# Performance work log

Hardware: AMD Instinct MI355X
Metric: run time of the kernel (lower is better)

Reference implementation:

```python
import jax, jax.numpy as jnp
import numpy as np

B, LC, LQ, H = 64, 1024, 128, 512
NEG = -1e30


def setup_inputs() -> dict:
    key = jax.random.key(0)
    ks = jax.random.split(key, 12)
    s = 1.0 / np.sqrt(H)
    return {
        "c": jax.random.normal(ks[0], (B, LC, H), jnp.float32),
        "q": jax.random.normal(ks[1], (B, LQ, H), jnp.float32),
        "c_mask": jax.random.randint(ks[2], (B, LC), 0, 2, jnp.int32),
        "q_mask": jax.random.randint(ks[3], (B, LQ), 0, 2, jnp.int32),
        "c_weight": jax.random.normal(ks[4], (H, 1), jnp.float32) * s,
        "q_weight": jax.random.normal(ks[5], (H, 1), jnp.float32) * s,
        "cq_weight": jax.random.normal(ks[6], (1, 1, H), jnp.float32) * s,
        "bias": jnp.zeros((1,), jnp.float32),
        "W1": jax.random.normal(ks[7], (H, H), jnp.float32) * s,
        "b1": jnp.zeros((H,), jnp.float32),
        "W2": jax.random.normal(ks[8], (H, H), jnp.float32) * s,
        "b2": jnp.zeros((H,), jnp.float32),
    }


def reference(c, q, c_mask, q_mask, c_weight, q_weight, cq_weight, bias, W1, b1, W2, b2):
    # --- trilinear similarity (BiDAF eq. 1, memory-efficient form) ---
    s0 = c @ c_weight                                   # [B, LC, 1]
    s1 = jnp.swapaxes(q @ q_weight, 1, 2)               # [B, 1, LQ]
    s2 = jnp.einsum('bch,bqh->bcq', c * cq_weight, q)   # [B, LC, LQ]
    sim = s0 + s1 + s2 + bias

    qm = (q_mask != 0)[:, None, :]   # [B, 1, LQ]
    cm = (c_mask != 0)[:, :, None]   # [B, LC, 1]

    # dual masked softmax (dropout is identity in eval mode)
    s1s = jax.nn.softmax(jnp.where(qm, sim, NEG), axis=2)  # c2q weights
    s2s = jax.nn.softmax(jnp.where(cm, sim, NEG), axis=1)  # q2c weights

    a = s1s @ q                                            # [B, LC, H]
    b = jnp.einsum('bcq,bkq->bck', s1s, s2s) @ c           # [B, LC, H]

    # co-attention branch: qprime = relu(lin2(relu(lin1(q))))
    qp = jax.nn.relu(jax.nn.relu(q @ W1 + b1) @ W2 + b2)   # [B, LQ, H]
    scoat = jnp.einsum('bch,bqh->bcq', c, qp)              # [B, LC, LQ]
    sc1 = jax.nn.softmax(jnp.where(qm, scoat, NEG), axis=2)
    sc2 = jax.nn.softmax(jnp.where(cm, scoat, NEG), axis=1)
    acoat = sc1 @ qp                                       # [B, LC, H]
    bcoat = jnp.einsum('bcq,bch->bqh', sc2, c)             # [B, LQ, H]
    scoat3 = sc1 @ bcoat                                   # [B, LC, H]

    return jnp.concatenate([c, a, c * a, c * b, scoat3, acoat], axis=2)  # [B, LC, 6H]
```

## Files before the change

### kernel.cpp

```cpp
#include <hip/hip_runtime.h>
#include <cstdint>
#include <cstddef>

typedef short    bf16x8 __attribute__((ext_vector_type(8)));
typedef _Float16 f16x8  __attribute__((ext_vector_type(8)));
typedef _Float16 f16x4  __attribute__((ext_vector_type(4)));
typedef float    f32x4  __attribute__((ext_vector_type(4)));

#define NEGV (-1e30f)
#define LDT 40

__device__ __forceinline__ short f2bf(float x){
    union { float f; unsigned u; } v; v.f = x;
    return (short)((v.u + 0x7fffu + ((v.u >> 16) & 1u)) >> 16);
}
__device__ __forceinline__ float bf2f(short h){
    union { float f; unsigned u; } v; v.u = ((unsigned)(unsigned short)h) << 16; return v.f;
}
__device__ __forceinline__ short f2h(float x){
    _Float16 h = (_Float16)x;
    union { _Float16 h; unsigned short u; } v; v.h = h;
    return (short)v.u;
}
__device__ __forceinline__ unsigned packh(float a, float b){
    return (unsigned)(unsigned short)f2h(a) | ((unsigned)(unsigned short)f2h(b) << 16);
}
__device__ __forceinline__ int p64(int x){ return ((x & 3) << 4) | (x >> 2); }

__global__ __launch_bounds__(256)
void k_prep_w(const float* __restrict__ W1, const float* __restrict__ W2,
              short* __restrict__ W1Th, short* __restrict__ W1Tl,
              short* __restrict__ W2Th, short* __restrict__ W2Tl)
{
    int idx = blockIdx.x * 256 + threadIdx.x;
    int w = idx >> 18;
    int e = idx & ((1 << 18) - 1);
    int n = e & 511, k = e >> 9;
    const float* W = w ? W2 : W1;
    float x = W[k * 512 + n];
    short hi = f2bf(x);
    short lo = f2bf(x - bf2f(hi));
    size_t o = (size_t)n * 512 + k;
    if (w) { W2Th[o] = hi; W2Tl[o] = lo; } else { W1Th[o] = hi; W1Tl[o] = lo; }
}

__global__ __launch_bounds__(256)
void k_prep_q(const float* __restrict__ q, const float* __restrict__ qwv,
              const float* __restrict__ cqw, short* __restrict__ q_cq,
              short* __restrict__ qT, float* __restrict__ s1p)
{
    __shared__ short TT[128 * 136];
    __shared__ float qws[128], cqs[128];
    const int t = threadIdx.x;
    const int b = (int)(blockIdx.x >> 2), hb = (int)(blockIdx.x & 3), h0 = hb * 128;
    if (t < 128) { qws[t] = qwv[h0 + t]; cqs[t] = cqw[h0 + t]; }
    __syncthreads();
    #pragma unroll
    for (int it = 0; it < 16; it++) {
        int idx = it * 256 + t;
        int m = idx >> 5, c4 = (idx & 31) * 4;
        float4 v = *(const float4*)(q + ((size_t)b * 128 + m) * 512 + h0 + c4);
        TT[(c4 + 0) * 136 + m] = f2h(v.x);
        TT[(c4 + 1) * 136 + m] = f2h(v.y);
        TT[(c4 + 2) * 136 + m] = f2h(v.z);
        TT[(c4 + 3) * 136 + m] = f2h(v.w);
        uint2 d;
        d.x = packh(v.x * cqs[c4],     v.y * cqs[c4 + 1]);
        d.y = packh(v.z * cqs[c4 + 2], v.w * cqs[c4 + 3]);
        *(uint2*)(q_cq + ((size_t)b * 128 + m) * 512 + h0 + c4) = d;
        float dot = v.x * qws[c4] + v.y * qws[c4 + 1] + v.z * qws[c4 + 2] + v.w * qws[c4 + 3];
        #pragma unroll
        for (int off = 1; off < 32; off <<= 1) dot += __shfl_xor(dot, off);
        if ((t & 31) == 0) s1p[((size_t)b * 4 + hb) * 128 + m] = dot;
    }
    __syncthreads();
    const int h = t >> 1, half = t & 1;
    const int hm = (h & 64) + p64(h & 63);
    short* dst = qT + ((size_t)b * 512 + h0 + hm) * 128 + half * 64;
    #pragma unroll
    for (int j = 0; j < 8; j++)
        *(bf16x8*)(dst + j * 8) = *(const bf16x8*)&TT[h * 136 + half * 64 + j * 8];
}

template<bool WT>
__global__ __launch_bounds__(256)
void k_linear(const float* __restrict__ X, const short* __restrict__ WTh,
              const short* __restrict__ WTl, const float* __restrict__ bias,
              float* __restrict__ Y, short* __restrict__ Yf,
              short* __restrict__ YT)
{
    __shared__ __align__(16) short SMEM[4 * 128 * LDT];
    short* Ah = SMEM;
    short* Al = SMEM + 128 * LDT;
    short* Bh = SMEM + 2 * 128 * LDT;
    short* Bl = SMEM + 3 * 128 * LDT;
    const int t = threadIdx.x;
    const int m0 = (int)(blockIdx.x >> 2) * 128;
    const int n0 = (int)(blockIdx.x & 3) * 128;
    const int lane = t & 63;
    const int wr = (t >> 7) & 1, wc = (t >> 6) & 1;
    const int fr = lane & 15, fg = lane >> 4;
    const int srow = t >> 1, sk = (t & 1) * 16;

    f32x4 acc[4][4] = {};

    float4 fX[4];
    bf16x8 fWh[2], fWl[2];
    bf16x8 hiR[2], loR[2];
    auto load_raw = [&](int k0) {
        const float* src = X + (size_t)(m0 + srow) * 512 + k0 + sk;
        #pragma unroll
        for (int i = 0; i < 4; i++) fX[i] = ((const float4*)src)[i];
        const short* sh = WTh + (size_t)(n0 + srow) * 512 + k0 + sk;
        const short* sl = WTl + (size_t)(n0 + srow) * 512 + k0 + sk;
        fWh[0] = ((const bf16x8*)sh)[0]; fWh[1] = ((const bf16x8*)sh)[1];
        fWl[0] = ((const bf16x8*)sl)[0]; fWl[1] = ((const bf16x8*)sl)[1];
    };
    auto split_cvt = [&]() {
        const float* fv = (const float*)fX;
        short hi[16], lo[16];
        #pragma unroll
        for (int j = 0; j < 16; j++) {
            float x = fv[j];
            short h = f2bf(x);
            hi[j] = h; lo[j] = f2bf(x - bf2f(h));
        }
        hiR[0] = *(bf16x8*)&hi[0]; hiR[1] = *(bf16x8*)&hi[8];
        loR[0] = *(bf16x8*)&lo[0]; loR[1] = *(bf16x8*)&lo[8];
    };

    load_raw(0);
    split_cvt();

    for (int k0 = 0; k0 < 512; k0 += 32) {
        __syncthreads();
        *(bf16x8*)&Ah[srow * LDT + sk]     = hiR[0];
        *(bf16x8*)&Ah[srow * LDT + sk + 8] = hiR[1];
        *(bf16x8*)&Al[srow * LDT + sk]     = loR[0];
        *(bf16x8*)&Al[srow * LDT + sk + 8] = loR[1];
        *(bf16x8*)&Bh[srow * LDT + sk]     = fWh[0];
        *(bf16x8*)&Bh[srow * LDT + sk + 8] = fWh[1];
        *(bf16x8*)&Bl[srow * LDT + sk]     = fWl[0];
        *(bf16x8*)&Bl[srow * LDT + sk + 8] = fWl[1];
        __syncthreads();
        const bool more = (k0 + 32) < 512;
        if (more) load_raw(k0 + 32);
        bf16x8 a_h[4], a_l[4], b_h[4], b_l[4];
        #pragma unroll
        for (int i = 0; i < 4; i++) {
            int ar = (wr * 64 + i * 16 + fr) * LDT + fg * 8;
            int br = (wc * 64 + i * 16 + fr) * LDT + fg * 8;
            a_h[i] = *(const bf16x8*)&Ah[ar];
            a_l[i] = *(const bf16x8*)&Al[ar];
            b_h[i] = *(const bf16x8*)&Bh[br];
            b_l[i] = *(const bf16x8*)&Bl[br];
        }
        #pragma unroll
        for (int mi = 0; mi < 4; mi++)
        #pragma unroll
        for (int ni = 0; ni < 4; ni++) {
            acc[mi][ni] = __builtin_amdgcn_mfma_f32_16x16x32_bf16(a_h[mi], b_h[ni], acc[mi][ni], 0, 0, 0);
            acc[mi][ni] = __builtin_amdgcn_mfma_f32_16x16x32_bf16(a_h[mi], b_l[ni], acc[mi][ni], 0, 0, 0);
            acc[mi][ni] = __builtin_amdgcn_mfma_f32_16x16x32_bf16(a_l[mi], b_h[ni], acc[mi][ni], 0, 0, 0);
        }
        if (more) split_cvt();
    }
    float bv[4];
    #pragma unroll
    for (int ni = 0; ni < 4; ni++) bv[ni] = bias[n0 + wc * 64 + ni * 16 + fr];

    if (!WT) {
        #pragma unroll
        for (int mi = 0; mi < 4; mi++)
        #pragma unroll
        for (int r = 0; r < 4; r++) {
            int row = m0 + wr * 64 + mi * 16 + fg * 4 + r;
            #pragma unroll
            for (int ni = 0; ni < 4; ni++)
                Y[(size_t)row * 512 + n0 + wc * 64 + ni * 16 + fr] =
                    fmaxf(acc[mi][ni][r] + bv[ni], 0.f);
        }
    } else {
        #pragma unroll
        for (int mi = 0; mi < 4; mi++)
        #pragma unroll
        for (int r = 0; r < 4; r++) {
            int row = m0 + wr * 64 + mi * 16 + fg * 4 + r;
            #pragma unroll
            for (int ni = 0; ni < 4; ni++) {
                float v = fmaxf(acc[mi][ni][r] + bv[ni], 0.f);
                size_t o = (size_t)row * 512 + n0 + wc * 64 + ni * 16 + fr;
                Yf[o] = f2h(v);
            }
        }
        __syncthreads();
        short* TT = SMEM;
        #pragma unroll
        for (int mi = 0; mi < 4; mi++)
        #pragma unroll
        for (int r = 0; r < 4; r++) {
            int ml = wr * 64 + mi * 16 + fg * 4 + r;
            #pragma unroll
            for (int ni = 0; ni < 4; ni++)
                TT[(wc * 64 + ni * 16 + fr) * 136 + ml] =
                    f2h(fmaxf(acc[mi][ni][r] + bv[ni], 0.f));
        }
        __syncthreads();
        const int n = t >> 1, half = t & 1;
        const int nm = (n & 64) + p64(n & 63);
        short* dst = YT + ((size_t)(m0 >> 7) * 512 + n0 + nm) * 128 + half * 64;
        #pragma unroll
        for (int j = 0; j < 8; j++)
            *(bf16x8*)(dst + j * 8) = *(const bf16x8*)&TT[n * 136 + half * 64 + j * 8];
    }
}

__global__ __launch_bounds__(256, 2)
void k_att_dual(const float* __restrict__ Cc, const short* __restrict__ B1g,
                const short* __restrict__ B2g, const float* __restrict__ cwv,
                const float* __restrict__ s1pg, const float* __restrict__ biasp,
                const int* __restrict__ qmask, const int* __restrict__ cmask,
                short* __restrict__ c16,
                short* __restrict__ Pr1, short* __restrict__ Pe1, float2* __restrict__ cp1,
                short* __restrict__ Pr2, short* __restrict__ Pe2, float2* __restrict__ cp2)
{
    __shared__ __align__(16) short SM[128 * 136];
    short* Ah  = SM;
    short* B1h = SM + 128 * LDT;
    short* B2h = SM + 2 * 128 * LDT;
    short* TT  = SM;
    __shared__ float red[2][128];
    __shared__ float mrowL[128], rinvL[128], cmaxL[128];
    __shared__ float cws[512];
    __shared__ float s0red[128][2];
    __shared__ float s0L[128], s1L[128];
    __shared__ int qmsL[128], cmsL[128];

    const int t = threadIdx.x;
    const int b  = (int)(blockIdx.x & 63);
    const int ch = (int)(blockIdx.x >> 6);
    const int m0 = ch * 128;
    const int lane = t & 63;
    const int wr = (t >> 7) & 1, wc = (t >> 6) & 1;
    const int fr = lane & 15, fg = lane >> 4;
    const int srow = t >> 1, sk = (t & 1) * 16;

    cws[t] = cwv[t]; cws[t + 256] = cwv[t + 256];
    if (t < 128) {
        qmsL[t] = qmask[b * 128 + t];
        cmsL[t] = cmask[b * 1024 + m0 + t];
        s1L[t] = s1pg[((size_t)b * 4 + 0) * 128 + t] + s1pg[((size_t)b * 4 + 1) * 128 + t]
               + s1pg[((size_t)b * 4 + 2) * 128 + t] + s1pg[((size_t)b * 4 + 3) * 128 + t];
    }

    const size_t aoff = ((size_t)b * 1024 + m0 + srow) * 512;
    const size_t boff = ((size_t)b * 128 + srow) * 512;
    float s0part = 0.f;
    f32x4 acc1[4][4] = {}, acc2[4][4] = {};

    float4 fA[4];
    uint4 fB1[2], fB2[2];
    bf16x8 hvR[2];
    auto load_raw = [&](int k0) {
        const float* src = Cc + aoff + k0 + sk;
        #pragma unroll
        for (int i = 0; i < 4; i++) fA[i] = ((const float4*)src)[i];
        fB1[0] = *(const uint4*)(B1g + boff + k0 + sk);
        fB1[1] = *(const uint4*)(B1g + boff + k0 + sk + 8);
        fB2[0] = *(const uint4*)(B2g + boff + k0 + sk);
        fB2[1] = *(const uint4*)(B2g + boff + k0 + sk + 8);
    };
    auto cvt_exp = [&](int k0) {
        const float* fv = (const float*)fA;
        short hv[16];
        #pragma unroll
        for (int j = 0; j < 16; j++) {
            float x = fv[j];
            s0part += x * cws[k0 + sk + j];
            hv[j] = f2h(x);
        }
        hvR[0] = *(bf16x8*)&hv[0]; hvR[1] = *(bf16x8*)&hv[8];
        *(bf16x8*)(c16 + aoff + k0 + sk)     = hvR[0];
        *(bf16x8*)(c16 + aoff + k0 + sk + 8) = hvR[1];
    };

    load_raw(0);
    cvt_exp(0);

    for (int k0 = 0; k0 < 512; k0 += 32) {
        __syncthreads();
        *(bf16x8*)&Ah[srow * LDT + sk]      = hvR[0];
        *(bf16x8*)&Ah[srow * LDT + sk + 8]  = hvR[1];
        *(uint4*)&B1h[srow * LDT + sk]      = fB1[0];
        *(uint4*)&B1h[srow * LDT + sk + 8]  = fB1[1];
        *(uint4*)&B2h[srow * LDT + sk]      = fB2[0];
        *(uint4*)&B2h[srow * LDT + sk + 8]  = fB2[1];
        __syncthreads();
        const bool more = (k0 + 32) < 512;
        if (more) load_raw(k0 + 32);
        #pragma unroll
        for (int i = 0; i < 4; i++) {
            f16x8 a_ = *(const f16x8*)&Ah[(wr * 64 + i * 16 + fr) * LDT + fg * 8];
            #pragma unroll
            for (int ni = 0; ni < 4; ni++) {
                int br = (wc * 64 + ni * 16 + fr) * LDT + fg * 8;
                f16x8 b1_ = *(const f16x8*)&B1h[br];
                acc1[i][ni] = __builtin_amdgcn_mfma_f32_16x16x32_f16(a_, b1_, acc1[i][ni], 0, 0, 0);
                f16x8 b2_ = *(const f16x8*)&B2h[br];
                acc2[i][ni] = __builtin_amdgcn_mfma_f32_16x16x32_f16(a_, b2_, acc2[i][ni], 0, 0, 0);
            }
        }
        if (more) cvt_exp(k0 + 32);
    }

    s0red[srow][t & 1] = s0part;
    __syncthreads();
    if (t < 128) s0L[t] = s0red[t][0] + s0red[t][1];
    __syncthreads();
    {
        float b0 = biasp[0];
        #pragma unroll
        for (int mi = 0; mi < 4; mi++)
        #pragma unroll
        for (int r = 0; r < 4; r++) {
            float s0r = s0L[wr * 64 + mi * 16 + fg * 4 + r] + b0;
            #pragma unroll
            for (int ni = 0; ni < 4; ni++)
                acc1[mi][ni][r] += s0r + s1L[wc * 64 + ni * 16 + fr];
        }
    }

    bool qmv[4];
    #pragma unroll
    for (int ni = 0; ni < 4; ni++) qmv[ni] = qmsL[wc * 64 + ni * 16 + fr] != 0;
    bool cmb[4][4];
    #pragma unroll
    for (int mi = 0; mi < 4; mi++)
    #pragma unroll
    for (int r = 0; r < 4; r++) cmb[mi][r] = cmsL[wr * 64 + mi * 16 + fg * 4 + r] != 0;

    auto emit = [&](f32x4 (&acc)[4][4], short* __restrict__ Pr,
                    short* __restrict__ Pe, float2* __restrict__ cpart_g) {
        __syncthreads();
        #pragma unroll
        for (int mi = 0; mi < 4; mi++)
        #pragma unroll
        for (int r = 0; r < 4; r++) {
            float m = NEGV;
            #pragma unroll
            for (int ni = 0; ni < 4; ni++) if (qmv[ni]) m = fmaxf(m, acc[mi][ni][r]);
            #pragma unroll
            for (int off = 1; off < 16; off <<= 1) m = fmaxf(m, __shfl_xor(m, off));
            if (fr == 0) red[wc][wr * 64 + mi * 16 + fg * 4 + r] = m;
        }
        __syncthreads();
        if (t < 128) mrowL[t] = fmaxf(red[0][t], red[1][t]);
        __syncthreads();
        #pragma unroll
        for (int mi = 0; mi < 4; mi++)
        #pragma unroll
        for (int r = 0; r < 4; r++) {
            float mr = mrowL[wr * 64 + mi * 16 + fg * 4 + r];
            float s = 0.f;
            #pragma unroll
            for (int ni = 0; ni < 4; ni++) if (qmv[ni]) s += __expf(acc[mi][ni][r] - mr);
            #pragma unroll
            for (int off = 1; off < 16; off <<= 1) s += __shfl_xor(s, off);
            if (fr == 0) red[wc][wr * 64 + mi * 16 + fg * 4 + r] = s;
        }
        __syncthreads();
        if (t < 128) rinvL[t] = 1.f / (red[0][t] + red[1][t]);
        __syncthreads();
        #pragma unroll
        for (int mi = 0; mi < 4; mi++)
        #pragma unroll
        for (int r = 0; r < 4; r++) {
            int rowl = wr * 64 + mi * 16 + fg * 4 + r;
            float mr = mrowL[rowl], iv = rinvL[rowl];
            size_t obase = ((size_t)b * 1024 + m0 + rowl) * 128;
            #pragma unroll
            for (int ni = 0; ni < 4; ni++) {
                float o = qmv[ni] ? __expf(acc[mi][ni][r] - mr) * iv : 0.f;
                Pr[obase + wc * 64 + ni * 16 + fr] = f2h(o);
            }
        }
        float cpart[4];
        #pragma unroll
        for (int ni = 0; ni < 4; ni++) {
            float m = NEGV;
            #pragma unroll
            for (int mi = 0; mi < 4; mi++)
            #pragma unroll
            for (int r = 0; r < 4; r++) if (cmb[mi][r]) m = fmaxf(m, acc[mi][ni][r]);
            m = fmaxf(m, __shfl_xor(m, 16));
            m = fmaxf(m, __shfl_xor(m, 32));
            cpart[ni] = m;
        }
        if (fg == 0) {
            #pragma unroll
            for (int ni = 0; ni < 4; ni++) red[wr][wc * 64 + ni * 16 + fr] = cpart[ni];
        }
        __syncthreads();
        if (t < 128) cmaxL[t] = fmaxf(red[0][t], red[1][t]);
        __syncthreads();
        #pragma unroll
        for (int ni = 0; ni < 4; ni++) {
            const int q = wc * 64 + ni * 16 + fr;
            float cm = cmaxL[q];
            float s = 0.f;
            #pragma unroll
            for (int mi = 0; mi < 4; mi++)
            #pragma unroll
            for (int r = 0; r < 4; r++) {
                int rloc = wr * 64 + mi * 16 + fg * 4 + r;
                float e = cmb[mi][r] ? __expf(acc[mi][ni][r] - cm) : 0.f;
                s += e;
                TT[q * 136 + rloc] = f2h(e);
            }
            s += __shfl_xor(s, 16);
            s += __shfl_xor(s, 32);
            cpart[ni] = s;
        }
        __syncthreads();
        if (fg == 0) {
            #pragma unroll
            for (int ni = 0; ni < 4; ni++) red[wr][wc * 64 + ni * 16 + fr] = cpart[ni];
        }
        __syncthreads();
        {
            const int q2 = t >> 1, half = t & 1;
            short* dst = Pe + ((size_t)b * 128 + q2) * 1024 + m0 + half * 64;
            #pragma unroll
            for (int j = 0; j < 8; j++)
                *(bf16x8*)(dst + j * 8) = *(const bf16x8*)&TT[q2 * 136 + half * 64 + j * 8];
        }
        if (t < 128) cpart_g[((size_t)b * 8 + ch) * 128 + t] = make_float2(cmaxL[t], red[0][t] + red[1][t]);
    };

    emit(acc1, Pr1, Pe1, cp1);
    emit(acc2, Pr2, Pe2, cp2);
}

__global__ __launch_bounds__(256)
void k_kgemm2(const short* __restrict__ A1, const short* __restrict__ A2,
              const short* __restrict__ C16, const float2* __restrict__ cpS,
              const float2* __restrict__ cpC, short* __restrict__ Y1T,
              short* __restrict__ Y2T)
{
    __shared__ __align__(16) short Bs[2][64 * LDT];
    __shared__ __align__(16) short TT[64 * 136];
    __shared__ float wtr[2][8][128];
    __shared__ float fin[2][128];
    const int t = threadIdx.x;
    const int b  = (int)(blockIdx.x & 63);
    const int n0 = (int)(blockIdx.x >> 6) * 64;
    const int lane = t & 63;
    const int w  = t >> 6;
    const int wr = w >> 1, wc = w & 1;
    const int fr = lane & 15, fg = lane >> 4;
    const int n4 = (t & 15) * 4, kk2 = (t >> 4) * 2;

    {
        const int tb = t >> 7, qq = t & 127;
        const float2* cp = tb ? cpC : cpS;
        float2 pc[8];
        #pragma unroll
        for (int c2 = 0; c2 < 8; c2++) pc[c2] = cp[((size_t)b * 8 + c2) * 128 + qq];
        float Mg = NEGV;
        #pragma unroll
        for (int c2 = 0; c2 < 8; c2++) Mg = fmaxf(Mg, pc[c2].x);
        float Sg = 0.f;
        #pragma unroll
        for (int c2 = 0; c2 < 8; c2++) Sg += pc[c2].y * __expf(pc[c2].x - Mg);
        const float clampv = Mg - 60.f;
        float mh[8];
        #pragma unroll
        for (int c2 = 0; c2 < 8; c2++) mh[c2] = fmaxf(pc[c2].x, clampv);
        wtr[tb][0][qq] = 1.f;
        #pragma unroll
        for (int c2 = 1; c2 < 8; c2++) wtr[tb][c2][qq] = __expf(mh[c2 - 1] - mh[c2]);
        fin[tb][qq] = (Sg > 0.f) ? __expf(mh[7] - Mg) / Sg : 0.f;
    }

    f32x4 acc1[4][2] = {}, acc2[4][2] = {};

    auto load_e = [&](int k0, uint2* e) {
        const short* p = C16 + ((size_t)b * 1024 + k0 + kk2) * 512 + n0 + n4;
        e[0] = *(const uint2*)(p);
        e[1] = *(const uint2*)(p + 512);
    };
    auto store_b = [&](const uint2* e, int buf) {
        const unsigned short* r0 = (const unsigned short*)&e[0];
        const unsigned short* r1 = (const unsigned short*)&e[1];
        #pragma unroll
        for (int l = 0; l < 4; l++)
            *(unsigned*)&Bs[buf][(n4 + l) * LDT + kk2] = (unsigned)r0[l] | ((unsigned)r1[l] << 16);
    };

    {
        uint2 e[2];
        load_e(0, e);
        store_b(e, 0);
    }
    __syncthreads();

    for (int k0 = 0; k0 < 1024; k0 += 32) {
        const int cur = (k0 >> 5) & 1;
        const bool more = (k0 + 32) < 1024;
        uint2 e[2];
        if (more) load_e(k0 + 32, e);
        if (k0 && (k0 & 127) == 0) {
            const int c2 = k0 >> 7;
            #pragma unroll
            for (int mi = 0; mi < 4; mi++)
            #pragma unroll
            for (int r = 0; r < 4; r++) {
                int qq = wr * 64 + mi * 16 + fg * 4 + r;
                float f1 = wtr[0][c2][qq], f2 = wtr[1][c2][qq];
                #pragma unroll
                for (int ni = 0; ni < 2; ni++) {
                    acc1[mi][ni][r] *= f1;
                    acc2[mi][ni][r] *= f2;
                }
            }
        }
        f16x8 a1[4], a2[4], bg[2];
        #pragma unroll
        for (int i = 0; i < 4; i++) {
            size_t arow = (size_t)(b * 128 + wr * 64 + i * 16 + fr) * 1024 + k0 + fg * 8;
            a1[i] = *(const f16x8*)(A1 + arow);
            a2[i] = *(const f16x8*)(A2 + arow);
        }
        #pragma unroll
        for (int i = 0; i < 2; i++)
            bg[i] = *(const f16x8*)&Bs[cur][(wc * 32 + i * 16 + fr) * LDT + fg * 8];
        #pragma unroll
        for (int mi = 0; mi < 4; mi++)
        #pragma unroll
        for (int ni = 0; ni < 2; ni++) {
            acc1[mi][ni] = __builtin_amdgcn_mfma_f32_16x16x32_f16(a1[mi], bg[ni], acc1[mi][ni], 0, 0, 0);
            acc2[mi][ni] = __builtin_amdgcn_mfma_f32_16x16x32_f16(a2[mi], bg[ni], acc2[mi][ni], 0, 0, 0);
        }
        if (more) store_b(e, cur ^ 1);
        __syncthreads();
    }

    const int n_l = t >> 2, qu = t & 3;
    const int nm = p64(n_l);
    #pragma unroll
    for (int mi = 0; mi < 4; mi++)
    #pragma unroll
    for (int r = 0; r < 4; r++) {
        int ml = wr * 64 + mi * 16 + fg * 4 + r;
        float fs = fin[0][ml];
        #pragma unroll
        for (int ni = 0; ni < 2; ni++)
            TT[(wc * 32 + ni * 16 + fr) * 136 + ml] = f2h(acc1[mi][ni][r] * fs);
    }
    __syncthreads();
    {
        short* dst = Y1T + ((size_t)b * 512 + n0 + nm) * 128 + qu * 32;
        #pragma unroll
        for (int j = 0; j < 4; j++)
            *(bf16x8*)(dst + j * 8) = *(const bf16x8*)&TT[n_l * 136 + qu * 32 + j * 8];
    }
    __syncthreads();
    #pragma unroll
    for (int mi = 0; mi < 4; mi++)
    #pragma unroll
    for (int r = 0; r < 4; r++) {
        int ml = wr * 64 + mi * 16 + fg * 4 + r;
        float fs = fin[1][ml];
        #pragma unroll
        for (int ni = 0; ni < 2; ni++)
            TT[(wc * 32 + ni * 16 + fr) * 136 + ml] = f2h(acc2[mi][ni][r] * fs);
    }
    __syncthreads();
    {
        short* dst = Y2T + ((size_t)b * 512 + n0 + nm) * 128 + qu * 32;
        #pragma unroll
        for (int j = 0; j < 4; j++)
            *(bf16x8*)(dst + j * 8) = *(const bf16x8*)&TT[n_l * 136 + qu * 32 + j * 8];
    }
}

template<bool WITHC>
__global__ __launch_bounds__(256)
void k_epi(const short* __restrict__ Pm, const short* __restrict__ BT1,
           const short* __restrict__ BT2, const short* __restrict__ C16,
           float* __restrict__ out)
{
    const int t = threadIdx.x;
    const int hb = (int)(blockIdx.x & 3);
    const int mb = (int)((blockIdx.x >> 2) & 7);
    const int b  = (int)(blockIdx.x >> 5);
    const int m0 = mb * 128, h0 = hb * 128;
    const int lane = t & 63;
    const int wr = (t >> 7) & 1, wc = (t >> 6) & 1;
    const int fr = lane & 15, fg = lane >> 4;
    f32x4 acc1[4][4] = {}, acc2[4][4] = {};
    const short* Abase  = Pm  + ((size_t)b * 1024 + m0) * 128;
    const short* B1base = BT1 + ((size_t)b * 512 + h0) * 128;
    const short* B2base = BT2 + ((size_t)b * 512 + h0) * 128;
    #pragma unroll
    for (int kk = 0; kk < 4; kk++) {
        const int k0 = kk * 32;
        f16x8 af[4], b1[4], b2[4];
        #pragma unroll
        for (int i = 0; i < 4; i++) {
            af[i] = *(const f16x8*)(Abase  + (size_t)(wr * 64 + i * 16 + fr) * 128 + k0 + fg * 8);
            b1[i] = *(const f16x8*)(B1base + (size_t)(wc * 64 + i * 16 + fr) * 128 + k0 + fg * 8);
            b2[i] = *(const f16x8*)(B2base + (size_t)(wc * 64 + i * 16 + fr) * 128 + k0 + fg * 8);
        }
        #pragma unroll
        for (int mi = 0; mi < 4; mi++)
        #pragma unroll
        for (int ni = 0; ni < 4; ni++) {
            acc1[mi][ni] = __builtin_amdgcn_mfma_f32_16x16x32_f16(af[mi], b1[ni], acc1[mi][ni], 0, 0, 0);
            acc2[mi][ni] = __builtin_amdgcn_mfma_f32_16x16x32_f16(af[mi], b2[ni], acc2[mi][ni], 0, 0, 0);
        }
    }
    const size_t crow_base = (size_t)b * 1024 + m0;
    const int colb = wc * 64 + fr * 4;
    #pragma unroll
    for (int mi = 0; mi < 4; mi++)
    #pragma unroll
    for (int r = 0; r < 4; r++) {
        int rowl = wr * 64 + mi * 16 + fg * 4 + r;
        size_t obase = (crow_base + rowl) * 3072 + h0 + colb;
        float4 av, bv;
        av.x = acc1[mi][0][r]; av.y = acc1[mi][1][r]; av.z = acc1[mi][2][r]; av.w = acc1[mi][3][r];
        bv.x = acc2[mi][0][r]; bv.y = acc2[mi][1][r]; bv.z = acc2[mi][2][r]; bv.w = acc2[mi][3][r];
        if (WITHC) {
            f16x4 cv4 = *(const f16x4*)(C16 + (crow_base + rowl) * 512 + h0 + colb);
            float4 cv;
            cv.x = (float)cv4[0]; cv.y = (float)cv4[1]; cv.z = (float)cv4[2]; cv.w = (float)cv4[3];
            *(float4*)(out + obase) = cv;
            *(float4*)(out + obase + 512) = av;
            float4 ca; ca.x = cv.x * av.x; ca.y = cv.y * av.y; ca.z = cv.z * av.z; ca.w = cv.w * av.w;
            *(float4*)(out + obase + 1024) = ca;
            float4 cb; cb.x = cv.x * bv.x; cb.y = cv.y * bv.y; cb.z = cv.z * bv.z; cb.w = cv.w * bv.w;
            *(float4*)(out + obase + 1536) = cb;
        } else {
            *(float4*)(out + obase + 2048) = bv;
            *(float4*)(out + obase + 2560) = av;
        }
    }
}

extern "C" void kernel_launch(void* const* d_in, const int* in_sizes, int n_in,
                              void* d_out, int out_size, void* d_ws, size_t ws_size,
                              hipStream_t stream)
{
    const float* c     = (const float*)d_in[0];
    const float* q     = (const float*)d_in[1];
    const int*   cmask = (const int*)d_in[2];
    const int*   qmask = (const int*)d_in[3];
    const float* cwv   = (const float*)d_in[4];
    const float* qwv   = (const float*)d_in[5];
    const float* cqw   = (const float*)d_in[6];
    const float* bias  = (const float*)d_in[7];
    const float* W1    = (const float*)d_in[8];
    const float* b1    = (const float*)d_in[9];
    const float* W2    = (const float*)d_in[10];
    const float* b2    = (const float*)d_in[11];
    float* out = (float*)d_out;

    char* ws = (char*)d_ws;
    size_t off = 0;
    auto alloc = [&](size_t bytes) -> char* {
        char* p = ws + off;
        off = (off + bytes + 255) & ~(size_t)255;
        return p;
    };
    short* w1th = (short*)alloc(512 * 512 * 2);
    short* w1tl = (short*)alloc(512 * 512 * 2);
    short* w2th = (short*)alloc(512 * 512 * 2);
    short* w2tl = (short*)alloc(512 * 512 * 2);
    float* s1p  = (float*)alloc(64 * 4 * 128 * 4);
    short* q_cq = (short*)alloc((size_t)64 * 128 * 512 * 2);
    short* qT   = (short*)alloc((size_t)64 * 512 * 128 * 2);
    float* z1   = (float*)alloc((size_t)8192 * 512 * 4);
    short* qp_f = (short*)alloc((size_t)8192 * 512 * 2);
    short* qpT  = (short*)alloc((size_t)64 * 512 * 128 * 2);
    short* c16  = (short*)alloc((size_t)64 * 1024 * 512 * 2);
    float2* colpartS = (float2*)alloc((size_t)64 * 8 * 128 * 8);
    float2* colpartC = (float2*)alloc((size_t)64 * 8 * 128 * 8);
    short* s1s  = (short*)alloc((size_t)64 * 1024 * 128 * 2);
    short* s2sT = (short*)alloc((size_t)64 * 128 * 1024 * 2);
    short* sc1  = (short*)alloc((size_t)64 * 1024 * 128 * 2);
    short* sc2T = (short*)alloc((size_t)64 * 128 * 1024 * 2);
    short* binT = (short*)z1;
    short* bcoT = ((short*)z1) + (size_t)64 * 512 * 128;

    k_prep_w<<<2048, 256, 0, stream>>>(W1, W2, w1th, w1tl, w2th, w2tl);
    k_prep_q<<<256, 256, 0, stream>>>(q, qwv, cqw, q_cq, qT, s1p);
    k_linear<false><<<256, 256, 0, stream>>>(q, w1th, w1tl, b1, z1, nullptr, nullptr);
    k_linear<true><<<256, 256, 0, stream>>>(z1, w2th, w2tl, b2, nullptr, qp_f, qpT);

    k_att_dual<<<512, 256, 0, stream>>>(
        c, q_cq, qp_f, cwv, s1p, bias, qmask, cmask, c16,
        s1s, s2sT, colpartS, sc1, sc2T, colpartC);

    k_kgemm2<<<512, 256, 0, stream>>>(s2sT, sc2T, c16, colpartS, colpartC, binT, bcoT);

    k_epi<true><<<2048, 256, 0, stream>>>(s1s, qT, binT, c16, out);
    k_epi<false><<<2048, 256, 0, stream>>>(sc1, qpT, bcoT, nullptr, out);
}
```

Baseline: 572.3 us.

## Merge epilogue GEMM kernels into one launch with smaller tiles and sequential accumulators

Replaces the two templated epilogue launches with a single kernel of 8192 blocks that picks the attention or co-attention branch from the low bit of the block index. The M tile is halved to 64 rows, and the two GEMMs per block run one after another, each with a 2x4 accumulator set instead of two simultaneous 4x4 sets. This cuts accumulator register pressure to raise occupancy, removes one launch, and lets both branches' stores interleave. In exchange the c16 tile is loaded twice in part 0 and the A fragments are reloaded for each GEMM.

```diff
diff --git a/kernel.cpp b/kernel.cpp
--- a/kernel.cpp
+++ b/kernel.cpp
@@ -584,66 +584,109 @@
     }
 }
 
-template<bool WITHC>
 __global__ __launch_bounds__(256)
-void k_epi(const short* __restrict__ Pm, const short* __restrict__ BT1,
-           const short* __restrict__ BT2, const short* __restrict__ C16,
-           float* __restrict__ out)
+void k_epi2(const short* __restrict__ s1s, const short* __restrict__ qT,
+            const short* __restrict__ binT, const short* __restrict__ c16,
+            const short* __restrict__ sc1, const short* __restrict__ qpT,
+            const short* __restrict__ bcoT, float* __restrict__ out)
 {
+    const int bid = (int)blockIdx.x;
+    const int part = bid & 1;
+    const int lb = bid >> 1;
+    const int hb = lb & 3, mb = (lb >> 2) & 15, b = lb >> 6;
+    const int m0 = mb * 64, h0 = hb * 128;
     const int t = threadIdx.x;
-    const int hb = (int)(blockIdx.x & 3);
-    const int mb = (int)((blockIdx.x >> 2) & 7);
-    const int b  = (int)(blockIdx.x >> 5);
-    const int m0 = mb * 128, h0 = hb * 128;
     const int lane = t & 63;
     const int wr = (t >> 7) & 1, wc = (t >> 6) & 1;
     const int fr = lane & 15, fg = lane >> 4;
-    f32x4 acc1[4][4] = {}, acc2[4][4] = {};
-    const short* Abase  = Pm  + ((size_t)b * 1024 + m0) * 128;
-    const short* B1base = BT1 + ((size_t)b * 512 + h0) * 128;
-    const short* B2base = BT2 + ((size_t)b * 512 + h0) * 128;
-    #pragma unroll
-    for (int kk = 0; kk < 4; kk++) {
-        const int k0 = kk * 32;
-        f16x8 af[4], b1[4], b2[4];
-        #pragma unroll
-        for (int i = 0; i < 4; i++) {
-            af[i] = *(const f16x8*)(Abase  + (size_t)(wr * 64 + i * 16 + fr) * 128 + k0 + fg * 8);
-            b1[i] = *(const f16x8*)(B1base + (size_t)(wc * 64 + i * 16 + fr) * 128 + k0 + fg * 8);
-            b2[i] = *(const f16x8*)(B2base + (size_t)(wc * 64 + i * 16 + fr) * 128 + k0 + fg * 8);
-        }
-        #pragma unroll
-        for (int mi = 0; mi < 4; mi++)
-        #pragma unroll
-        for (int ni = 0; ni < 4; ni++) {
-            acc1[mi][ni] = __builtin_amdgcn_mfma_f32_16x16x32_f16(af[mi], b1[ni], acc1[mi][ni], 0, 0, 0);
-            acc2[mi][ni] = __builtin_amdgcn_mfma_f32_16x16x32_f16(af[mi], b2[ni], acc2[mi][ni], 0, 0, 0);
-        }
-    }
+
+    const short* Abase  = (part ? sc1  : s1s) + ((size_t)b * 1024 + m0) * 128;
+    const short* B1base = (part ? bcoT : qT)   + ((size_t)b * 512 + h0) * 128;
+    const short* B2base = (part ? qpT  : binT) + ((size_t)b * 512 + h0) * 128;
+
+    auto gemm = [&](const short* Bb, f32x4 (&acc)[2][4]) {
+        #pragma unroll
+        for (int kk = 0; kk < 4; kk++) {
+            const int k0 = kk * 32;
+            f16x8 af[2], bf[4];
+            #pragma unroll
+            for (int mi = 0; mi < 2; mi++)
+                af[mi] = *(const f16x8*)(Abase + (size_t)(wr * 32 + mi * 16 + fr) * 128 + k0 + fg * 8);
+            #pragma unroll
+            for (int ni = 0; ni < 4; ni++)
+                bf[ni] = *(const f16x8*)(Bb + (size_t)(wc * 64 + ni * 16 + fr) * 128 + k0 + fg * 8);
+            #pragma unroll
+            for (int mi = 0; mi < 2; mi++)
+            #pragma unroll
+            for (int ni = 0; ni < 4; ni++)
+                acc[mi][ni] = __builtin_amdgcn_mfma_f32_16x16x32_f16(af[mi], bf[ni], acc[mi][ni], 0, 0, 0);
+        }
+    };
+
     const size_t crow_base = (size_t)b * 1024 + m0;
     const int colb = wc * 64 + fr * 4;
-    #pragma unroll
-    for (int mi = 0; mi < 4; mi++)
-    #pragma unroll
-    for (int r = 0; r < 4; r++) {
-        int rowl = wr * 64 + mi * 16 + fg * 4 + r;
-        size_t obase = (crow_base + rowl) * 3072 + h0 + colb;
-        float4 av, bv;
-        av.x = acc1[mi][0][r]; av.y = acc1[mi][1][r]; av.z = acc1[mi][2][r]; av.w = acc1[mi][3][r];
-        bv.x = acc2[mi][0][r]; bv.y = acc2[mi][1][r]; bv.z = acc2[mi][2][r]; bv.w = acc2[mi][3][r];
-        if (WITHC) {
-            f16x4 cv4 = *(const f16x4*)(C16 + (crow_base + rowl) * 512 + h0 + colb);
-            float4 cv;
-            cv.x = (float)cv4[0]; cv.y = (float)cv4[1]; cv.z = (float)cv4[2]; cv.w = (float)cv4[3];
-            *(float4*)(out + obase) = cv;
-            *(float4*)(out + obase + 512) = av;
-            float4 ca; ca.x = cv.x * av.x; ca.y = cv.y * av.y; ca.z = cv.z * av.z; ca.w = cv.w * av.w;
-            *(float4*)(out + obase + 1024) = ca;
-            float4 cb; cb.x = cv.x * bv.x; cb.y = cv.y * bv.y; cb.z = cv.z * bv.z; cb.w = cv.w * bv.w;
-            *(float4*)(out + obase + 1536) = cb;
-        } else {
-            *(float4*)(out + obase + 2048) = bv;
-            *(float4*)(out + obase + 2560) = av;
+
+    if (part == 0) {
+        {
+            f32x4 acc[2][4] = {};
+            gemm(B1base, acc);
+            #pragma unroll
+            for (int mi = 0; mi < 2; mi++)
+            #pragma unroll
+            for (int r = 0; r < 4; r++) {
+                int rowl = wr * 32 + mi * 16 + fg * 4 + r;
+                size_t obase = (crow_base + rowl) * 3072 + h0 + colb;
+                f16x4 cv4 = *(const f16x4*)(c16 + (crow_base + rowl) * 512 + h0 + colb);
+                float4 cv; cv.x = (float)cv4[0]; cv.y = (float)cv4[1]; cv.z = (float)cv4[2]; cv.w = (float)cv4[3];
+                float4 av; av.x = acc[mi][0][r]; av.y = acc[mi][1][r]; av.z = acc[mi][2][r]; av.w = acc[mi][3][r];
+                *(float4*)(out + obase) = cv;
+                *(float4*)(out + obase + 512) = av;
+                float4 ca; ca.x = cv.x * av.x; ca.y = cv.y * av.y; ca.z = cv.z * av.z; ca.w = cv.w * av.w;
+                *(float4*)(out + obase + 1024) = ca;
+            }
+        }
+        {
+            f32x4 acc[2][4] = {};
+            gemm(B2base, acc);
+            #pragma unroll
+            for (int mi = 0; mi < 2; mi++)
+            #pragma unroll
+            for (int r = 0; r < 4; r++) {
+                int rowl = wr * 32 + mi * 16 + fg * 4 + r;
+                size_t obase = (crow_base + rowl) * 3072 + h0 + colb;
+                f16x4 cv4 = *(const f16x4*)(c16 + (crow_base + rowl) * 512 + h0 + colb);
+                float4 cv; cv.x = (float)cv4[0]; cv.y = (float)cv4[1]; cv.z = (float)cv4[2]; cv.w = (float)cv4[3];
+                float4 bv; bv.x = acc[mi][0][r]; bv.y = acc[mi][1][r]; bv.z = acc[mi][2][r]; bv.w = acc[mi][3][r];
+                float4 cb; cb.x = cv.x * bv.x; cb.y = cv.y * bv.y; cb.z = cv.z * bv.z; cb.w = cv.w * bv.w;
+                *(float4*)(out + obase + 1536) = cb;
+            }
+        }
+    } else {
+        {
+            f32x4 acc[2][4] = {};
+            gemm(B1base, acc);
+            #pragma unroll
+            for (int mi = 0; mi < 2; mi++)
+            #pragma unroll
+            for (int r = 0; r < 4; r++) {
+                int rowl = wr * 32 + mi * 16 + fg * 4 + r;
+                size_t obase = (crow_base + rowl) * 3072 + h0 + colb;
+                float4 v; v.x = acc[mi][0][r]; v.y = acc[mi][1][r]; v.z = acc[mi][2][r]; v.w = acc[mi][3][r];
+                *(float4*)(out + obase + 2048) = v;
+            }
+        }
+        {
+            f32x4 acc[2][4] = {};
+            gemm(B2base, acc);
+            #pragma unroll
+            for (int mi = 0; mi < 2; mi++)
+            #pragma unroll
+            for (int r = 0; r < 4; r++) {
+                int rowl = wr * 32 + mi * 16 + fg * 4 + r;
+                size_t obase = (crow_base + rowl) * 3072 + h0 + colb;
+                float4 v; v.x = acc[mi][0][r]; v.y = acc[mi][1][r]; v.z = acc[mi][2][r]; v.w = acc[mi][3][r];
+                *(float4*)(out + obase + 2560) = v;
+            }
         }
     }
 }
@@ -704,6 +747,5 @@
 
     k_kgemm2<<<512, 256, 0, stream>>>(s2sT, sc2T, c16, colpartS, colpartC, binT, bcoT);
 
-    k_epi<true><<<2048, 256, 0, stream>>>(s1s, qT, binT, c16, out);
-    k_epi<false><<<2048, 256, 0, stream>>>(sc1, qpT, bcoT, nullptr, out);
-}
+    k_epi2<<<8192, 256, 0, stream>>>(s1s, qT, binT, c16, sc1, qpT, bcoT, out);
+}
```

After: 628.5 us. 1.1x slower.
